# Kernel tuning notes

Measured on AMD Instinct MI355X. Metric: run time of the kernel, lower is better.

Reference implementation:

```python
import jax, jax.numpy as jnp
import numpy as np

B, TQ, TK, D, H = 8, 1024, 1024, 1024, 16
HD = D // H
EPS = 1e-5


def layernorm(x, g, b):
    mu = jnp.mean(x, axis=-1, keepdims=True)
    var = jnp.mean(jnp.square(x - mu), axis=-1, keepdims=True)
    return (x - mu) * jax.lax.rsqrt(var + EPS) * g + b


def setup_inputs() -> dict:
    key = jax.random.key(0)
    ks = jax.random.split(key, 16)
    s = 1.0 / np.sqrt(D)
    return {
        "base": jax.random.normal(ks[0], (B, TQ, D), jnp.float32),
        "fusion": jax.random.normal(ks[1], (B, TK, D), jnp.float32),
        "Wq": jax.random.normal(ks[2], (D, D), jnp.float32) * s,
        "Wk": jax.random.normal(ks[3], (D, D), jnp.float32) * s,
        "Wv": jax.random.normal(ks[4], (D, D), jnp.float32) * s,
        "Wo": jax.random.normal(ks[5], (D, D), jnp.float32) * s,
        "g1": jnp.ones((D,), jnp.float32),
        "b1": jnp.zeros((D,), jnp.float32),
        "g2": jnp.ones((D,), jnp.float32),
        "b2": jnp.zeros((D,), jnp.float32),
        "fc1_w": jax.random.normal(ks[6], (D, D), jnp.float32) * s,
        "fc1_b": jnp.zeros((D,), jnp.float32),
        "fc2_w": jax.random.normal(ks[7], (D, D), jnp.float32) * s,
        "fc2_b": jnp.zeros((D,), jnp.float32),
        "rw": jax.random.normal(ks[8], (D, D), jnp.float32) * s,
        "rb": jnp.zeros((D,), jnp.float32),
        "alpha": jnp.asarray(0.1, jnp.float32),
    }


def reference(base, fusion, Wq, Wk, Wv, Wo, g1, b1, g2, b2,
              fc1_w, fc1_b, fc2_w, fc2_b, rw, rb, alpha):
    def split_heads(x):  # [B,T,D] -> [B,H,T,hd]
        return x.reshape(B, -1, H, HD).transpose(0, 2, 1, 3)

    Q = split_heads(base @ Wq.T)
    K = split_heads(fusion @ Wk.T)
    V = split_heads(fusion @ Wv.T)

    scores = jnp.einsum("bhqd,bhkd->bhqk", Q, K) / jnp.sqrt(jnp.float32(HD))
    attn = jax.nn.softmax(scores, axis=-1)
    # threshold mask (the torch scatter_ with arange indices is an identity copy)
    masked = attn * (attn >= alpha).astype(attn.dtype)
    # second softmax over masked weights (zeros contribute exp(0)=1, as in the original)
    attn2 = jax.nn.softmax(masked, axis=-1)
    out = jnp.einsum("bhqk,bhkd->bhqd", attn2, V)
    out = out.transpose(0, 2, 1, 3).reshape(B, TQ, D)
    out = out @ Wo.T
    x = layernorm(base + out, g1, b1)  # dropout is eval-mode identity
    ff = jax.nn.silu(jax.nn.silu(x @ fc1_w.T + fc1_b) @ fc2_w.T + fc2_b)
    y = layernorm(x + ff, g2, b2)
    final = y @ rw.T + rb
    return final, masked
```

## Files before the change

### kernel.cpp

```cpp
#include <hip/hip_runtime.h>


typedef unsigned short u16;
typedef __attribute__((ext_vector_type(8))) short  bf16x8;
typedef __attribute__((ext_vector_type(4))) float  f32x4;

#define GLL16(gp, lp) __builtin_amdgcn_global_load_lds(                     \
    (__attribute__((address_space(1))) const void*)(gp),                    \
    (__attribute__((address_space(3))) void*)(lp), 16, 0, 0)

__device__ __forceinline__ u16 f2bf(float x) {
  union { float f; unsigned u; } v; v.f = x;
  return (u16)((v.u + 0x7FFF + ((v.u >> 16) & 1)) >> 16);
}
__device__ __forceinline__ float bf2f(u16 h) {
  union { unsigned u; float f; } v; v.u = ((unsigned)h) << 16;
  return v.f;
}
__device__ __forceinline__ f32x4 zero4() { f32x4 z = {0.f, 0.f, 0.f, 0.f}; return z; }

__global__ __launch_bounds__(256) void pack_act(const float* __restrict__ a,
                                                const float* __restrict__ b,
                                                u16* __restrict__ outa,
                                                u16* __restrict__ outb) {
  size_t i = (size_t)blockIdx.x * 256 + threadIdx.x;
  const float* in = blockIdx.y ? b : a;
  u16* out = blockIdx.y ? outb : outa;
  out[i] = f2bf(in[i]);
}

__global__ __launch_bounds__(256) void pack_w(
    const float* __restrict__ w0, const float* __restrict__ w1,
    const float* __restrict__ w2, const float* __restrict__ w3,
    const float* __restrict__ w4, const float* __restrict__ w5,
    const float* __restrict__ w6, u16* __restrict__ out) {
  size_t i = (size_t)blockIdx.x * 256 + threadIdx.x;
  const float* in;
  switch (blockIdx.y) {
    case 0: in = w0; break;  case 1: in = w1; break;
    case 2: in = w2; break;  case 3: in = w3; break;
    case 4: in = w4; break;  case 5: in = w5; break;
    default: in = w6; break;
  }
  out[(size_t)blockIdx.y * 1048576 + i] = f2bf(in[i]);
}

#define EPI_QKV       0
#define EPI_BF16      1
#define EPI_SILU_BF16 4
#define EPI_BIAS_F32  6

template <int EPI>
__global__ __launch_bounds__(256) void gemm_bt(
    const u16* __restrict__ A, int lda,
    const u16* __restrict__ W, int ldw,
    int M, int N, int K,
    float* __restrict__ outF, u16* __restrict__ outU,
    const float* __restrict__ bias,
    const u16* __restrict__ A2) {
  __shared__ u16 As[2][128 * 32];
  __shared__ u16 Bs[2][128 * 32];
  int tid = threadIdx.x;
  int l = tid & 63, w = tid >> 6;
  int wr = w >> 1, wc = w & 1, lr = l & 15, lq = l >> 4;
  int m0 = blockIdx.y * 128, n0 = blockIdx.x * 128;

  const u16* Ap = A;
  const u16* Wp = W;
  u16* outUp = outU;
  if constexpr (EPI == EPI_QKV) {
    int z = blockIdx.z;
    if (z) Ap = A2;
    Wp = W + (size_t)z * 1048576;
    outUp = outU + (size_t)z * 8388608;
  }

  f32x4 acc[4][4];
#pragma unroll
  for (int i = 0; i < 4; i++)
#pragma unroll
    for (int j = 0; j < 4; j++) acc[i][j] = zero4();

  auto stage = [&](const u16* src, int ld, int r0, int k0, u16* lds) {
#pragma unroll
    for (int j = 0; j < 2; ++j) {
      int seg = j * 256 + tid;
      int row = seg >> 2, sp = seg & 3;
      const u16* g = src + (size_t)(r0 + row) * ld + k0 +
                     ((sp ^ ((row >> 1) & 3)) << 3);
      GLL16(g, lds + seg * 8);
    }
  };

  int nk = K >> 5;
  stage(Ap, lda, m0, 0, As[0]);
  stage(Wp, ldw, n0, 0, Bs[0]);
  for (int kt = 0; kt < nk; ++kt) {
    __syncthreads();
    if (kt + 1 < nk) {
      stage(Ap, lda, m0, (kt + 1) << 5, As[(kt + 1) & 1]);
      stage(Wp, ldw, n0, (kt + 1) << 5, Bs[(kt + 1) & 1]);
    }
    const u16* Ab = As[kt & 1];
    const u16* Bb = Bs[kt & 1];
    bf16x8 af[4], bw[4];
    int slot = (lq ^ ((lr >> 1) & 3)) << 3;
#pragma unroll
    for (int mi = 0; mi < 4; mi++)
      af[mi] = *(const bf16x8*)&Ab[(wr * 64 + mi * 16 + lr) * 32 + slot];
#pragma unroll
    for (int ni = 0; ni < 4; ni++)
      bw[ni] = *(const bf16x8*)&Bb[(wc * 64 + ni * 16 + lr) * 32 + slot];
#pragma unroll
    for (int mi = 0; mi < 4; mi++)
#pragma unroll
      for (int ni = 0; ni < 4; ni++)
        acc[mi][ni] = __builtin_amdgcn_mfma_f32_16x16x32_bf16(af[mi], bw[ni],
                                                              acc[mi][ni], 0, 0, 0);
  }

#pragma unroll
  for (int mi = 0; mi < 4; mi++) {
#pragma unroll
    for (int ni = 0; ni < 4; ni++) {
      int col = n0 + wc * 64 + ni * 16 + lr;
#pragma unroll
      for (int r = 0; r < 4; r++) {
        int row = m0 + wr * 64 + mi * 16 + lq * 4 + r;
        float v = acc[mi][ni][r];
        if constexpr (EPI == EPI_QKV) {
          int b = row >> 10, t = row & 1023, h = col >> 6, d = col & 63;
          int z = blockIdx.z;
          if (z == 0) {
            outUp[((size_t)(b * 16 + h) * 1024 + t) * 64 + d] = f2bf(v);
          } else if (z == 1) {
            size_t base = ((size_t)(b * 16 + h) * 1024 + t) * 64;
            outUp[base + (((d >> 3) ^ (t & 7)) << 3) + (d & 7)] = f2bf(v);
          } else {
            size_t o = ((size_t)(b * 16 + h) * 64 + d) * 1024 + (t & ~63) +
                       ((((t >> 3) & 7) ^ (d & 7)) << 3) + (t & 7);
            outUp[o] = f2bf(v);
          }
        } else if constexpr (EPI == EPI_BF16) {
          outUp[(size_t)row * N + col] = f2bf(v);
        } else if constexpr (EPI == EPI_SILU_BF16) {
          float z = v + bias[col];
          outUp[(size_t)row * N + col] = f2bf(z / (1.f + __expf(-z)));
        } else {
          outF[(size_t)row * N + col] = v + bias[col];
        }
      }
    }
  }
}

__global__ __launch_bounds__(256) void attn_kernel(
    const u16* __restrict__ Q2, const u16* __restrict__ K2,
    const u16* __restrict__ Vt, const float* __restrict__ alphap,
    float* __restrict__ masked_out, u16* __restrict__ attn_out) {
  __shared__ __align__(16) u16 Ks[2][4096];
  __shared__ __align__(16) u16 Vs[2][4096];
  __shared__ __align__(16) u16 Ps[4][2][16 * 72];

  int tid = threadIdx.x;
  int l = tid & 63, w = tid >> 6, lr = l & 15, lq = l >> 4;
  int q0 = blockIdx.x * 128;
  int h = blockIdx.y, b = blockIdx.z;
  int bh = b * 16 + h;
  const u16* Qb = Q2 + (size_t)bh * 1024 * 64;
  const u16* Kb = K2 + (size_t)bh * 1024 * 64;
  const u16* Vb = Vt + (size_t)bh * 64 * 1024;
  float alpha = alphap[0];
  int qw = q0 + w * 32;

  auto stageK = [&](int kc, u16* dst) {
#pragma unroll
    for (int j = 0; j < 2; ++j) {
      int seg = j * 256 + tid;
      GLL16(Kb + (size_t)kc * 4096 + seg * 8, dst + seg * 8);
    }
  };
  auto stageV = [&](int kc, u16* dst) {
#pragma unroll
    for (int j = 0; j < 2; ++j) {
      int seg = j * 256 + tid;
      GLL16(Vb + (size_t)(seg >> 3) * 1024 + kc * 64 + (seg & 7) * 8, dst + seg * 8);
    }
  };

  bf16x8 qf[2][2];
#pragma unroll
  for (int s = 0; s < 2; s++)
#pragma unroll
    for (int kt = 0; kt < 2; kt++)
      qf[s][kt] = *(const bf16x8*)(Qb + (size_t)(qw + s * 16 + lr) * 64 + kt * 32 + lq * 8);

  float s1[2][4] = {{0.f, 0.f, 0.f, 0.f}, {0.f, 0.f, 0.f, 0.f}};

  stageK(0, Ks[0]);
  for (int kc = 0; kc < 16; ++kc) {
    __syncthreads();
    if (kc + 1 < 16) stageK(kc + 1, Ks[(kc + 1) & 1]);
    const u16* Kc = Ks[kc & 1];
    f32x4 acc[2][4];
#pragma unroll
    for (int s = 0; s < 2; s++)
#pragma unroll
      for (int ni = 0; ni < 4; ni++) acc[s][ni] = zero4();
#pragma unroll
    for (int ni = 0; ni < 4; ++ni) {
      int t = ni * 16 + lr;
      bf16x8 k0 = *(const bf16x8*)&Kc[t * 64 + (((0 + lq) ^ (lr & 7)) << 3)];
      bf16x8 k1 = *(const bf16x8*)&Kc[t * 64 + (((4 + lq) ^ (lr & 7)) << 3)];
#pragma unroll
      for (int s = 0; s < 2; s++) {
        acc[s][ni] = __builtin_amdgcn_mfma_f32_16x16x32_bf16(qf[s][0], k0, acc[s][ni], 0, 0, 0);
        acc[s][ni] = __builtin_amdgcn_mfma_f32_16x16x32_bf16(qf[s][1], k1, acc[s][ni], 0, 0, 0);
      }
    }
#pragma unroll
    for (int s = 0; s < 2; s++)
#pragma unroll
      for (int ni = 0; ni < 4; ni++)
#pragma unroll
        for (int r = 0; r < 4; r++)
          s1[s][r] += __expf(acc[s][ni][r] * 0.125f);
  }
#pragma unroll
  for (int s = 0; s < 2; s++)
#pragma unroll
    for (int r = 0; r < 4; r++) {
      float v = s1[s][r];
      v += __shfl_xor(v, 1); v += __shfl_xor(v, 2);
      v += __shfl_xor(v, 4); v += __shfl_xor(v, 8);
      s1[s][r] = 1.0f / v;
    }

  float s2[2][4] = {{0.f, 0.f, 0.f, 0.f}, {0.f, 0.f, 0.f, 0.f}};
  f32x4 oacc[2][4];
#pragma unroll
  for (int s = 0; s < 2; s++)
#pragma unroll
    for (int dg = 0; dg < 4; dg++) oacc[s][dg] = zero4();

  stageK(0, Ks[0]);
  stageV(0, Vs[0]);
  for (int kc = 0; kc < 16; ++kc) {
    if (kc == 0) {
      asm volatile("s_waitcnt vmcnt(0) lgkmcnt(0)" ::: "memory");
    } else {
      asm volatile("s_waitcnt vmcnt(32) lgkmcnt(0)" ::: "memory");
    }
    __builtin_amdgcn_s_barrier();
    __builtin_amdgcn_sched_barrier(0);
    if (kc + 1 < 16) {
      stageK(kc + 1, Ks[(kc + 1) & 1]);
      stageV(kc + 1, Vs[(kc + 1) & 1]);
    }
    const u16* Kc = Ks[kc & 1];
    const u16* Vc = Vs[kc & 1];

    f32x4 acc[2][4];
#pragma unroll
    for (int s = 0; s < 2; s++)
#pragma unroll
      for (int ni = 0; ni < 4; ni++) acc[s][ni] = zero4();
#pragma unroll
    for (int ni = 0; ni < 4; ++ni) {
      int t = ni * 16 + lr;
      bf16x8 k0 = *(const bf16x8*)&Kc[t * 64 + (((0 + lq) ^ (lr & 7)) << 3)];
      bf16x8 k1 = *(const bf16x8*)&Kc[t * 64 + (((4 + lq) ^ (lr & 7)) << 3)];
#pragma unroll
      for (int s = 0; s < 2; s++) {
        acc[s][ni] = __builtin_amdgcn_mfma_f32_16x16x32_bf16(qf[s][0], k0, acc[s][ni], 0, 0, 0);
        acc[s][ni] = __builtin_amdgcn_mfma_f32_16x16x32_bf16(qf[s][1], k1, acc[s][ni], 0, 0, 0);
      }
    }

#pragma unroll
    for (int s = 0; s < 2; s++) {
#pragma unroll
      for (int ni = 0; ni < 4; ni++) {
#pragma unroll
        for (int r = 0; r < 4; r++) {
          float e = __expf(acc[s][ni][r] * 0.125f);
          float a = e * s1[s][r];
          a = (a >= alpha) ? a : 0.0f;
          size_t row = (size_t)bh * 1024 + qw + s * 16 + lq * 4 + r;
          masked_out[row * 1024 + kc * 64 + ni * 16 + lr] = a;
          float p = __expf(a);
          s2[s][r] += p;
          Ps[w][s][(lq * 4 + r) * 72 + ni * 16 + lr] = f2bf(p);
        }
      }
    }
    asm volatile("s_waitcnt lgkmcnt(0)" ::: "memory");

    bf16x8 pf[2][2];
#pragma unroll
    for (int s = 0; s < 2; s++)
#pragma unroll
      for (int kt = 0; kt < 2; kt++)
        pf[s][kt] = *(const bf16x8*)&Ps[w][s][lr * 72 + kt * 32 + lq * 8];
#pragma unroll
    for (int dg = 0; dg < 4; dg++) {
      int d = dg * 16 + lr;
      bf16x8 v0 = *(const bf16x8*)&Vc[d * 64 + (((0 + lq) ^ (lr & 7)) << 3)];
      bf16x8 v1 = *(const bf16x8*)&Vc[d * 64 + (((4 + lq) ^ (lr & 7)) << 3)];
#pragma unroll
      for (int s = 0; s < 2; s++) {
        oacc[s][dg] = __builtin_amdgcn_mfma_f32_16x16x32_bf16(pf[s][0], v0, oacc[s][dg], 0, 0, 0);
        oacc[s][dg] = __builtin_amdgcn_mfma_f32_16x16x32_bf16(pf[s][1], v1, oacc[s][dg], 0, 0, 0);
      }
    }
  }

#pragma unroll
  for (int s = 0; s < 2; s++)
#pragma unroll
    for (int r = 0; r < 4; r++) {
      float v = s2[s][r];
      v += __shfl_xor(v, 1); v += __shfl_xor(v, 2);
      v += __shfl_xor(v, 4); v += __shfl_xor(v, 8);
      s2[s][r] = 1.0f / v;
    }
#pragma unroll
  for (int s = 0; s < 2; s++)
#pragma unroll
    for (int dg = 0; dg < 4; dg++)
#pragma unroll
      for (int r = 0; r < 4; r++) {
        int q = qw + s * 16 + lq * 4 + r;
        attn_out[(size_t)(b * 1024 + q) * 1024 + h * 64 + dg * 16 + lr] =
            f2bf(oacc[s][dg][r] * s2[s][r]);
      }
}

__global__ __launch_bounds__(256) void ln_kernel(
    const float* __restrict__ A, const u16* __restrict__ Bv,
    const float* __restrict__ g, const float* __restrict__ beta,
    float* __restrict__ outF, u16* __restrict__ outB) {
  __shared__ float red[4];
  int row = blockIdx.x, t = threadIdx.x;
  const float* pa = A + (size_t)row * 1024;
  const u16* pb = Bv + (size_t)row * 1024;
  float v[4];
  float s = 0.f;
#pragma unroll
  for (int i = 0; i < 4; i++) {
    int c = t + 256 * i;
    v[i] = pa[c] + bf2f(pb[c]);
    s += v[i];
  }
#pragma unroll
  for (int off = 1; off < 64; off <<= 1) s += __shfl_xor(s, off);
  if ((t & 63) == 0) red[t >> 6] = s;
  __syncthreads();
  s = red[0] + red[1] + red[2] + red[3];
  float mu = s * 0.0009765625f;
  float q = 0.f;
#pragma unroll
  for (int i = 0; i < 4; i++) { float d = v[i] - mu; q += d * d; }
  __syncthreads();
#pragma unroll
  for (int off = 1; off < 64; off <<= 1) q += __shfl_xor(q, off);
  if ((t & 63) == 0) red[t >> 6] = q;
  __syncthreads();
  q = red[0] + red[1] + red[2] + red[3];
  float rs = rsqrtf(q * 0.0009765625f + 1e-5f);
#pragma unroll
  for (int i = 0; i < 4; i++) {
    int c = t + 256 * i;
    float y = (v[i] - mu) * rs * g[c] + beta[c];
    if (outF) outF[(size_t)row * 1024 + c] = y;
    if (outB) outB[(size_t)row * 1024 + c] = f2bf(y);
  }
}

#define WS_BASEB   0
#define WS_FUSB    16777216
#define WS_W       33554432
#define WS_QKV     48234496
#define WS_ATTNO   98566144
#define WS_X       115343360
#define WS_OB      WS_FUSB
#define WS_XB      WS_BASEB
#define WS_H1      WS_ATTNO
#define WS_FFB     WS_QKV
#define WS_YB      (WS_QKV + 16777216)

extern "C" void kernel_launch(void* const* d_in, const int* in_sizes, int n_in,
                              void* d_out, int out_size, void* d_ws, size_t ws_size,
                              hipStream_t stream) {
  const float* base   = (const float*)d_in[0];
  const float* fusion = (const float*)d_in[1];
  const float* Wq     = (const float*)d_in[2];
  const float* Wk     = (const float*)d_in[3];
  const float* Wv     = (const float*)d_in[4];
  const float* Wo     = (const float*)d_in[5];
  const float* g1     = (const float*)d_in[6];
  const float* b1     = (const float*)d_in[7];
  const float* g2     = (const float*)d_in[8];
  const float* b2     = (const float*)d_in[9];
  const float* fc1w   = (const float*)d_in[10];
  const float* fc1b   = (const float*)d_in[11];
  const float* fc2w   = (const float*)d_in[12];
  const float* fc2b   = (const float*)d_in[13];
  const float* rw     = (const float*)d_in[14];
  const float* rb     = (const float*)d_in[15];
  const float* alphap = (const float*)d_in[16];

  char* ws = (char*)d_ws;
  u16* baseb  = (u16*)(ws + WS_BASEB);
  u16* fusb   = (u16*)(ws + WS_FUSB);
  u16* wall   = (u16*)(ws + WS_W);
  u16* Q2     = (u16*)(ws + WS_QKV);
  u16* attno  = (u16*)(ws + WS_ATTNO);
  u16* obufb  = (u16*)(ws + WS_OB);
  float* x    = (float*)(ws + WS_X);
  u16* xb     = (u16*)(ws + WS_XB);
  u16* h1     = (u16*)(ws + WS_H1);
  u16* ffb    = (u16*)(ws + WS_FFB);
  u16* yb     = (u16*)(ws + WS_YB);

  float* final_out  = (float*)d_out;
  float* masked_out = final_out + 8388608;

  pack_act<<<dim3(32768, 2), 256, 0, stream>>>(base, fusion, baseb, fusb);
  pack_w<<<dim3(4096, 7), 256, 0, stream>>>(Wq, Wk, Wv, Wo, fc1w, fc2w, rw, wall);

  dim3 gg(8, 64);

  gemm_bt<EPI_QKV><<<dim3(8, 64, 3), 256, 0, stream>>>(
      baseb, 1024, wall, 1024, 8192, 1024, 1024, nullptr, Q2, nullptr, fusb);

  attn_kernel<<<dim3(8, 16, 8), 256, 0, stream>>>(
      Q2, Q2 + 8388608, Q2 + 16777216, alphap, masked_out, attno);

  gemm_bt<EPI_BF16><<<gg, 256, 0, stream>>>(attno, 1024, wall + 3 * 1048576, 1024,
                                            8192, 1024, 1024, nullptr, obufb, nullptr, nullptr);
  ln_kernel<<<8192, 256, 0, stream>>>(base, obufb, g1, b1, x, xb);

  gemm_bt<EPI_SILU_BF16><<<gg, 256, 0, stream>>>(xb, 1024, wall + 4 * 1048576, 1024,
                                                 8192, 1024, 1024, nullptr, h1, fc1b, nullptr);
  gemm_bt<EPI_SILU_BF16><<<gg, 256, 0, stream>>>(h1, 1024, wall + 5 * 1048576, 1024,
                                                 8192, 1024, 1024, nullptr, ffb, fc2b, nullptr);
  ln_kernel<<<8192, 256, 0, stream>>>(x, ffb, g2, b2, nullptr, yb);

  gemm_bt<EPI_BIAS_F32><<<gg, 256, 0, stream>>>(yb, 1024, wall + 6 * 1048576, 1024,
                                                8192, 1024, 1024, final_out, nullptr, rb, nullptr);
}
```

Before: 1.041 ms.

## Vectorize pack kernels, swizzle GEMM/attention block order, raise MFMA priority

The fp32-to-bf16 pack kernels now load four floats and store four bf16 values per thread, so their grids shrink by a factor of four. GEMM tiles are remapped so that consecutively dispatched blocks spread across N tiles and M rows, which is meant to change L2 reuse across XCDs. The attention grid becomes one dimension, with block IDs remapped so neighbouring blocks land on different batch-heads. The MFMA sections are wrapped in s_setprio to favour matrix issue over other waves, at the risk of changing contention without a net benefit.

```diff
diff --git a/kernel.cpp b/kernel.cpp
--- a/kernel.cpp
+++ b/kernel.cpp
@@ -3,6 +3,7 @@
 
 typedef unsigned short u16;
 typedef __attribute__((ext_vector_type(8))) short  bf16x8;
+typedef __attribute__((ext_vector_type(4))) short  s16x4;
 typedef __attribute__((ext_vector_type(4))) float  f32x4;
 
 #define GLL16(gp, lp) __builtin_amdgcn_global_load_lds(                     \
@@ -24,9 +25,13 @@
                                                 u16* __restrict__ outa,
                                                 u16* __restrict__ outb) {
   size_t i = (size_t)blockIdx.x * 256 + threadIdx.x;
-  const float* in = blockIdx.y ? b : a;
-  u16* out = blockIdx.y ? outb : outa;
-  out[i] = f2bf(in[i]);
+  const f32x4* in = (const f32x4*)(blockIdx.y ? b : a);
+  s16x4* out = (s16x4*)(blockIdx.y ? outb : outa);
+  f32x4 v = in[i];
+  s16x4 o;
+  o[0] = (short)f2bf(v[0]); o[1] = (short)f2bf(v[1]);
+  o[2] = (short)f2bf(v[2]); o[3] = (short)f2bf(v[3]);
+  out[i] = o;
 }
 
 __global__ __launch_bounds__(256) void pack_w(
@@ -42,7 +47,11 @@
     case 4: in = w4; break;  case 5: in = w5; break;
     default: in = w6; break;
   }
-  out[(size_t)blockIdx.y * 1048576 + i] = f2bf(in[i]);
+  f32x4 v = ((const f32x4*)in)[i];
+  s16x4 o;
+  o[0] = (short)f2bf(v[0]); o[1] = (short)f2bf(v[1]);
+  o[2] = (short)f2bf(v[2]); o[3] = (short)f2bf(v[3]);
+  ((s16x4*)(out + (size_t)blockIdx.y * 1048576))[i] = o;
 }
 
 #define EPI_QKV       0
@@ -63,7 +72,10 @@
   int tid = threadIdx.x;
   int l = tid & 63, w = tid >> 6;
   int wr = w >> 1, wc = w & 1, lr = l & 15, lq = l >> 4;
-  int m0 = blockIdx.y * 128, n0 = blockIdx.x * 128;
+
+  int fid = blockIdx.y * 8 + blockIdx.x;
+  int swz = (fid & 7) * 64 + (fid >> 3);
+  int m0 = (swz >> 3) * 128, n0 = (swz & 7) * 128;
 
   const u16* Ap = A;
   const u16* Wp = W;
@@ -164,9 +176,13 @@
 
   int tid = threadIdx.x;
   int l = tid & 63, w = tid >> 6, lr = l & 15, lq = l >> 4;
-  int q0 = blockIdx.x * 128;
-  int h = blockIdx.y, b = blockIdx.z;
-  int bh = b * 16 + h;
+
+  int bid = blockIdx.x;
+  int qi  = bid >> 7;
+  int bh  = (bid & 7) * 16 + ((bid >> 3) & 15);
+  int h = bh & 15, b = bh >> 4;
+  int q0 = qi * 128;
+
   const u16* Qb = Q2 + (size_t)bh * 1024 * 64;
   const u16* Kb = K2 + (size_t)bh * 1024 * 64;
   const u16* Vb = Vt + (size_t)bh * 64 * 1024;
@@ -207,6 +223,7 @@
     for (int s = 0; s < 2; s++)
 #pragma unroll
       for (int ni = 0; ni < 4; ni++) acc[s][ni] = zero4();
+    __builtin_amdgcn_s_setprio(1);
 #pragma unroll
     for (int ni = 0; ni < 4; ++ni) {
       int t = ni * 16 + lr;
@@ -218,6 +235,7 @@
         acc[s][ni] = __builtin_amdgcn_mfma_f32_16x16x32_bf16(qf[s][1], k1, acc[s][ni], 0, 0, 0);
       }
     }
+    __builtin_amdgcn_s_setprio(0);
 #pragma unroll
     for (int s = 0; s < 2; s++)
 #pragma unroll
@@ -265,6 +283,7 @@
     for (int s = 0; s < 2; s++)
 #pragma unroll
       for (int ni = 0; ni < 4; ni++) acc[s][ni] = zero4();
+    __builtin_amdgcn_s_setprio(1);
 #pragma unroll
     for (int ni = 0; ni < 4; ++ni) {
       int t = ni * 16 + lr;
@@ -276,6 +295,7 @@
         acc[s][ni] = __builtin_amdgcn_mfma_f32_16x16x32_bf16(qf[s][1], k1, acc[s][ni], 0, 0, 0);
       }
     }
+    __builtin_amdgcn_s_setprio(0);
 
 #pragma unroll
     for (int s = 0; s < 2; s++) {
@@ -302,6 +322,7 @@
 #pragma unroll
       for (int kt = 0; kt < 2; kt++)
         pf[s][kt] = *(const bf16x8*)&Ps[w][s][lr * 72 + kt * 32 + lq * 8];
+    __builtin_amdgcn_s_setprio(1);
 #pragma unroll
     for (int dg = 0; dg < 4; dg++) {
       int d = dg * 16 + lr;
@@ -313,6 +334,7 @@
         oacc[s][dg] = __builtin_amdgcn_mfma_f32_16x16x32_bf16(pf[s][1], v1, oacc[s][dg], 0, 0, 0);
       }
     }
+    __builtin_amdgcn_s_setprio(0);
   }
 
 #pragma unroll
@@ -426,15 +448,15 @@
   float* final_out  = (float*)d_out;
   float* masked_out = final_out + 8388608;
 
-  pack_act<<<dim3(32768, 2), 256, 0, stream>>>(base, fusion, baseb, fusb);
-  pack_w<<<dim3(4096, 7), 256, 0, stream>>>(Wq, Wk, Wv, Wo, fc1w, fc2w, rw, wall);
+  pack_act<<<dim3(8192, 2), 256, 0, stream>>>(base, fusion, baseb, fusb);
+  pack_w<<<dim3(1024, 7), 256, 0, stream>>>(Wq, Wk, Wv, Wo, fc1w, fc2w, rw, wall);
 
   dim3 gg(8, 64);
 
   gemm_bt<EPI_QKV><<<dim3(8, 64, 3), 256, 0, stream>>>(
       baseb, 1024, wall, 1024, 8192, 1024, 1024, nullptr, Q2, nullptr, fusb);
 
-  attn_kernel<<<dim3(8, 16, 8), 256, 0, stream>>>(
+  attn_kernel<<<dim3(1024), 256, 0, stream>>>(
       Q2, Q2 + 8388608, Q2 + 16777216, alphap, masked_out, attno);
 
   gemm_bt<EPI_BF16><<<gg, 256, 0, stream>>>(attno, 1024, wall + 3 * 1048576, 1024,
```

After: 990.9 us. -4.8%, faster.
